# Performance work log

Hardware: AMD Instinct MI355X
Metric: run time of the kernel (lower is better)

The kernel has to match this reference:

```python
import jax, jax.numpy as jnp
import numpy as np

PATCH = 3
PAD = (PATCH - 1) // 2
WEIGHT = 100.0
EPS = 1e-9


def _extract_patches(fm):
    # fm: (C, H, W) -> (H*W, C*9) row i*W+j is the reflect-padded 3x3 patch at (i, j)
    C, H, W = fm.shape
    fm_pad = jnp.pad(fm, ((0, 0), (PAD, PAD), (PAD, PAD)), mode='reflect')
    shifts = [fm_pad[:, dh:dh + H, dw:dw + W] for dh in range(PATCH) for dw in range(PATCH)]
    p = jnp.stack(shifts, axis=0)            # (9, C, H, W)
    return p.reshape(PATCH * PATCH * C, H * W).T  # (HW, 9C)


def _match_fm(content_fm, style_fm):
    # content_fm, style_fm: (1, C, H, W); returns matched style fm (1,C,H,W) and idx (2,H,W)
    C, H, W = content_fm.shape[1:]
    cp = _extract_patches(content_fm[0])     # (HW, 9C) content patches (conv kernels)
    sp = _extract_patches(style_fm[0])       # (HW, 9C) style patches (conv sliding windows)
    c_norm = jnp.sqrt(jnp.sum(cp * cp, axis=1))  # kernel_norm per content location
    s_norm = jnp.sqrt(jnp.sum(sp * sp, axis=1))  # style_fm_norm per style location
    score = cp @ sp.T                            # (HW, HW) cross-correlation
    score = score / (c_norm[:, None] * s_norm[None, :] + EPS)
    idx = jnp.argmax(score, axis=1)              # flat argmax == torch.argmax on (H,W) map
    style_flat = style_fm[0].reshape(C, H * W)
    corr = style_flat[:, idx].reshape(1, C, H, W)  # gather matched style pixels
    corr_idx = jnp.stack([idx // W, idx % W], axis=0).reshape(2, H, W)
    return corr, corr_idx


def _masked_gram(fm, mask_flat, mask_sum):
    # fm: (1, C, H, W), mask_flat: (HW,) -> (C, C) gram of masked fm / sum(mask)
    C = fm.shape[1]
    f = fm[0].reshape(C, -1) * mask_flat[None, :]
    return (f @ f.T) / mask_sum


def setup_inputs() -> dict:
    key = jax.random.key(0)
    k1, k2, k3, k4 = jax.random.split(key, 4)
    B, C, H, W = 1, 512, 64, 64
    return {
        'content_fm': jax.random.normal(k1, (B, C, H, W), dtype=jnp.float32),
        'style_fm': jax.random.normal(k2, (B, C, H, W), dtype=jnp.float32),
        'input_fm': jax.random.normal(k3, (B, C, H, W), dtype=jnp.float32),
        'mask': jax.random.uniform(k4, (B, 1, H, W), dtype=jnp.float32),
    }


def reference(content_fm, style_fm, input_fm, mask):
    H, W = content_fm.shape[2:]
    mask_flat = mask[0, 0].reshape(H * W)
    mask_sum = jnp.sum(mask)
    # capture_style_ref: patch-match style fm to content fm, build target gram
    corr_fm, _ = _match_fm(content_fm, style_fm)
    target_gram = _masked_gram(corr_fm, mask_flat, mask_sum)
    # loss mode: masked gram of current image fm vs target, MSE (mean) * weight
    G = _masked_gram(input_fm, mask_flat, mask_sum)
    loss = jnp.mean((G - target_gram) ** 2) * WEIGHT
    return loss
```

## Files before the change

kernel.cpp:

```cpp
#include <hip/hip_runtime.h>

static constexpr int C  = 512;
static constexpr int P  = 4096;

typedef _Float16 half8  __attribute__((ext_vector_type(8)));
typedef float    f32x4  __attribute__((ext_vector_type(4)));

__device__ __forceinline__ int refl(int q) { return q < 0 ? 1 : (q > 63 ? 62 : q); }

__device__ __forceinline__ void g2l16(const void* g, const void* l) {
    __builtin_amdgcn_global_load_lds((const __attribute__((address_space(1))) unsigned int*)g,
                                     (__attribute__((address_space(3))) unsigned int*)l, 16, 0, 0);
}

__global__ __launch_bounds__(256) void k_prep(const float* __restrict__ content, const float* __restrict__ style,
                                              _Float16* __restrict__ Ah, _Float16* __restrict__ Bh,
                                              float* __restrict__ sqn_part, float* __restrict__ msum) {
    __shared__ float T[64][65];
    __shared__ float R4[4][64];
    if (blockIdx.x == 0 && threadIdx.x == 0) msum[0] = 0.f;
    const int p0 = (blockIdx.x & 63) * 64, c0 = (blockIdx.x >> 6) * 64;
    const int pl = threadIdx.x & 63, cq = threadIdx.x >> 6;
    const int pv = threadIdx.x >> 3;
    const int cv = (threadIdx.x & 7) * 8;

    #pragma unroll
    for (int r = 0; r < 16; ++r)
        T[cq + r * 4][pl] = content[(size_t)(c0 + cq + r * 4) * P + p0 + pl];
    __syncthreads();
    #pragma unroll
    for (int r = 0; r < 2; ++r) {
        int pl2 = pv + r * 32;
        half8 v;
        #pragma unroll
        for (int u = 0; u < 8; ++u) v[u] = (_Float16)T[cv + u][pl2];
        *(half8*)(Ah + (size_t)(p0 + pl2) * C + c0 + cv) = v;
    }
    __syncthreads();

    float sq = 0.f;
    #pragma unroll
    for (int r = 0; r < 16; ++r) {
        float v = style[(size_t)(c0 + cq + r * 4) * P + p0 + pl];
        T[cq + r * 4][pl] = v;
        sq += v * v;
    }
    R4[cq][pl] = sq;
    __syncthreads();
    if (cq == 0)
        sqn_part[(size_t)(blockIdx.x >> 6) * P + p0 + pl] = R4[0][pl] + R4[1][pl] + R4[2][pl] + R4[3][pl];
    #pragma unroll
    for (int r = 0; r < 2; ++r) {
        int pl2 = pv + r * 32;
        half8 v;
        #pragma unroll
        for (int u = 0; u < 8; ++u) v[u] = (_Float16)T[cv + u][pl2];
        *(half8*)(Bh + (size_t)(p0 + pl2) * C + c0 + cv) = v;
    }
}

__global__ __launch_bounds__(512, 2) void k_gemm16(const _Float16* __restrict__ Ah,
                                                   const _Float16* __restrict__ Bh,
                                                   float* __restrict__ Eo,
                                                   const float* __restrict__ sqn_part,
                                                   const float* __restrict__ mask,
                                                   float* __restrict__ inv_sn,
                                                   float* __restrict__ msum) {
    __shared__ _Float16 SH[65536];
    const int tid = threadIdx.x;
    const int bid = blockIdx.x;
    const int swz = (bid & 7) * 32 + (bid >> 3);
    const int by = swz >> 4, bx = swz & 15;

    {
        float* fsh = (float*)SH;
        const int jw0 = (bid * 16) & 63;
        const int ihh = (bid * 16) >> 6;
        if (tid < 432) {
            const int k = tid & 7, idx = tid >> 3;
            const int t3 = idx / 18, s = idx % 18;
            const int gr = refl(ihh - 1 + t3);
            const int jw = refl(jw0 - 1 + s);
            fsh[tid] = sqn_part[(size_t)k * P + gr * 64 + jw];
        }
        if (tid >= 480 && tid < 496) fsh[432 + tid - 480] = mask[bid * 16 + (tid - 480)];
        __syncthreads();
        if (tid < 54) {
            float s = fsh[tid * 8];
            #pragma unroll
            for (int k = 1; k < 8; ++k) s += fsh[tid * 8 + k];
            fsh[448 + tid] = s;
        }
        __syncthreads();
        if (tid < 16) {
            const float* sq = fsh + 448;
            float s2 = 0.f;
            #pragma unroll
            for (int t3 = 0; t3 < 3; ++t3)
                #pragma unroll
                for (int dd = 0; dd < 3; ++dd)
                    s2 += sq[t3 * 18 + tid + dd];
            inv_sn[bid * 16 + tid] = 1.0f / sqrtf(s2);
        }
        if (tid == 63) {
            float s = fsh[432];
            #pragma unroll
            for (int i = 1; i < 16; ++i) s += fsh[432 + i];
            atomicAdd(msum, s);
        }
        __syncthreads();
    }

    const int wave = tid >> 6, lane = tid & 63;
    const int wr = wave >> 2, wc = wave & 3;
    const int quad = lane >> 4, l15 = lane & 15;
    const int i0 = by * 256, j0 = bx * 256;

    const int r2 = tid >> 2;
    const int gofs = ((tid & 3) ^ (r2 & 3)) * 8;
    const _Float16* pA0 = Ah + (size_t)(i0 + r2) * C + gofs;
    const _Float16* pA1 = pA0 + (size_t)128 * C;
    const _Float16* pB0 = Bh + (size_t)(j0 + r2) * C + gofs;
    const _Float16* pB1 = pB0 + (size_t)128 * C;
    const int stw0 = wave * 512;
    const int stw1 = 4096 + wave * 512;

    const int aslot = (quad ^ (l15 & 3)) * 8;
    int aoff[8], boff[4];
    #pragma unroll
    for (int mi = 0; mi < 8; ++mi) aoff[mi] = (wr * 128 + mi * 16 + l15) * 32 + aslot;
    #pragma unroll
    for (int ni = 0; ni < 4; ++ni) boff[ni] = (wc * 64 + ni * 16 + l15) * 32 + aslot;

    f32x4 acc[8][4] = {};
    half8 af[8], bf0, bf1, bf2, bf3;

#define LDSA(b,k) (SH + (b) * 16384 + (k) * 8192)
#define LDSB(b,k) (SH + 32768 + (b) * 16384 + (k) * 8192)
#define STAGE_A(b,k,KC) do { g2l16(pA0 + (KC) + (k) * 32, LDSA(b,k) + stw0); \
                             g2l16(pA1 + (KC) + (k) * 32, LDSA(b,k) + stw1); } while (0)
#define STAGE_B(b,k,KC) do { g2l16(pB0 + (KC) + (k) * 32, LDSB(b,k) + stw0); \
                             g2l16(pB1 + (KC) + (k) * 32, LDSB(b,k) + stw1); } while (0)
#define READ_NP0(b,k) do { _Pragma("unroll") for (int mi = 0; mi < 8; ++mi) \
                               af[mi] = *(const half8*)(LDSA(b,k) + aoff[mi]); \
                           bf0 = *(const half8*)(LDSB(b,k) + boff[0]); \
                           bf1 = *(const half8*)(LDSB(b,k) + boff[1]); } while (0)
#define READ_NP1(b,k) do { bf2 = *(const half8*)(LDSB(b,k) + boff[2]); \
                           bf3 = *(const half8*)(LDSB(b,k) + boff[3]); } while (0)
#define MF8(BF,NI) do { _Pragma("unroll") for (int mi = 0; mi < 8; ++mi) \
    acc[mi][NI] = __builtin_amdgcn_mfma_f32_16x16x32_f16(af[mi], BF, acc[mi][NI], 0, 0, 0); } while (0)
#define WAITV4 asm volatile("s_waitcnt vmcnt(4)" ::: "memory")
#define WAITV0 asm volatile("s_waitcnt vmcnt(0)" ::: "memory")
#define EXEC16(B0,N0,B1,N1) do { \
    __builtin_amdgcn_s_barrier(); \
    asm volatile("s_waitcnt lgkmcnt(0)" ::: "memory"); \
    __builtin_amdgcn_sched_barrier(0); \
    __builtin_amdgcn_s_setprio(1); \
    MF8(B0, N0); MF8(B1, N1); \
    __builtin_amdgcn_s_setprio(0); \
    __builtin_amdgcn_s_barrier(); } while (0)

    STAGE_A(0, 0, 0); STAGE_B(0, 0, 0); STAGE_A(0, 1, 0); STAGE_B(0, 1, 0);
    WAITV4;
    __builtin_amdgcn_s_barrier();

    for (int it = 0; it < 4; ++it) {
        const int kk = it * 128;
        const bool nl = (it < 3);
        READ_NP0(0, 0); STAGE_A(1, 0, kk + 64);          EXEC16(bf0, 0, bf1, 1);
        READ_NP1(0, 0); STAGE_B(1, 0, kk + 64); WAITV4;  EXEC16(bf2, 2, bf3, 3);
        READ_NP0(0, 1); STAGE_A(1, 1, kk + 64);          EXEC16(bf0, 0, bf1, 1);
        READ_NP1(0, 1); STAGE_B(1, 1, kk + 64); WAITV4;  EXEC16(bf2, 2, bf3, 3);
        READ_NP0(1, 0); if (nl) STAGE_A(0, 0, kk + 128);
        EXEC16(bf0, 0, bf1, 1);
        READ_NP1(1, 0); if (nl) { STAGE_B(0, 0, kk + 128); WAITV4; } else { WAITV0; }
        EXEC16(bf2, 2, bf3, 3);
        READ_NP0(1, 1); if (nl) STAGE_A(0, 1, kk + 128);
        EXEC16(bf0, 0, bf1, 1);
        READ_NP1(1, 1); if (nl) { STAGE_B(0, 1, kk + 128); WAITV4; }
        EXEC16(bf2, 2, bf3, 3);
    }

#undef LDSA
#undef LDSB
#undef STAGE_A
#undef STAGE_B
#undef READ_NP0
#undef READ_NP1
#undef MF8
#undef WAITV4
#undef WAITV0
#undef EXEC16

    float* SHF = (float*)SH;
    __syncthreads();
    #pragma unroll
    for (int h = 0; h < 2; ++h) {
        if (wr == h) {
            #pragma unroll
            for (int mi = 0; mi < 8; ++mi) {
                const int row = mi * 16 + quad * 4;
                #pragma unroll
                for (int ni = 0; ni < 4; ++ni) {
                    float* W = SHF + row * 131 + wc * 64 + ni * 16 + l15;
                    W[0]   = acc[mi][ni][0];
                    W[131] = acc[mi][ni][1];
                    W[262] = acc[mi][ni][2];
                    W[393] = acc[mi][ni][3];
                }
            }
        }
        __syncthreads();
        {
            const int er  = tid >> 2;
            const int c00 = (tid & 3) * 8;
            const int ew  = er & 63;
            const int rm  = (er & 64) | (ew == 0 ? 1 : ew - 1);
            const int rp  = (er & 64) | (ew == 63 ? 62 : ew + 1);
            const float* Rm = SHF + rm * 131;
            const float* Rc = SHF + er * 131;
            const float* Rp = SHF + rp * 131;
            float* outRow = Eo + (size_t)(i0 + h * 128 + er) * P + j0;
            #pragma unroll
            for (int cc = 0; cc < 256; cc += 32) {
                const int cb  = c00 + cc;
                const int cw0 = cb & 63;
                f32x4 w0, w1;
                #pragma unroll
                for (int u = 0; u < 8; ++u) {
                    int cm = cb - 1 + u, cp = cb + 1 + u;
                    if (u == 0 && cw0 == 0)  cm = cb + 1;
                    if (u == 7 && cw0 == 56) cp = cb + 6;
                    float ev = Rm[cm] + Rc[cb + u] + Rp[cp];
                    if (u < 4) w0[u] = ev; else w1[u - 4] = ev;
                }
                *(f32x4*)(outRow + cb)     = w0;
                *(f32x4*)(outRow + cb + 4) = w1;
            }
        }
        if (h == 0) __syncthreads();
    }
}

__global__ __launch_bounds__(256) void k_argmax(const float* __restrict__ E,
                                                const float* __restrict__ inv_sn,
                                                int* __restrict__ idxOut) {
    const int i = blockIdx.x;
    const int ih = i >> 6, iw = i & 63;
    const int wave = threadIdx.x >> 6, l = threadIdx.x & 63, l15 = l & 15;
    size_t rb0 = (size_t)(refl(ih - 1) * 64 + iw) * P;
    size_t rb1 = (size_t)(ih * 64 + iw) * P;
    size_t rb2 = (size_t)(refl(ih + 1) * 64 + iw) * P;

    float best = -1e30f;
    int bidx = 0;
    #pragma unroll
    for (int s = 0; s < 4; ++s) {
        const int j0 = (wave * 4 + s) * 256 + l * 4;
        const int jh = j0 >> 6, jw0 = l15 * 4;
        const int cb0 = ((jh == 0) ? 1 : jh - 1) * 64 + jw0;
        const int cb1 = jh * 64 + jw0;
        const int cb2 = ((jh == 63) ? 62 : jh + 1) * 64 + jw0;
        f32x4 u0 = *(const f32x4*)(E + rb0 + cb0);
        f32x4 u1 = *(const f32x4*)(E + rb1 + cb1);
        f32x4 u2 = *(const f32x4*)(E + rb2 + cb2);
        float f0 = u0[0] + u1[0] + u2[0];
        float f1 = u0[1] + u1[1] + u2[1];
        float f2 = u0[2] + u1[2] + u2[2];
        float f3 = u0[3] + u1[3] + u2[3];
        const float4 is = *(const float4*)(inv_sn + j0);
        float v0 = f0 * is.x, v1 = f1 * is.y, v2 = f2 * is.z, v3 = f3 * is.w;
        if (v0 > best) { best = v0; bidx = j0; }
        if (v1 > best) { best = v1; bidx = j0 + 1; }
        if (v2 > best) { best = v2; bidx = j0 + 2; }
        if (v3 > best) { best = v3; bidx = j0 + 3; }
    }

    __shared__ float bv[256];
    __shared__ int   bi[256];
    bv[threadIdx.x] = best;
    bi[threadIdx.x] = bidx;
    __syncthreads();
    for (int t = 128; t > 0; t >>= 1) {
        if (threadIdx.x < t) {
            float ov = bv[threadIdx.x + t];
            int   oi = bi[threadIdx.x + t];
            if (ov > bv[threadIdx.x] || (ov == bv[threadIdx.x] && oi < bi[threadIdx.x])) {
                bv[threadIdx.x] = ov;
                bi[threadIdx.x] = oi;
            }
        }
        __syncthreads();
    }
    if (threadIdx.x == 0) idxOut[i] = bi[0];
}

__global__ __launch_bounds__(256) void k_build(const _Float16* __restrict__ Bh,
                                               const float* __restrict__ input,
                                               const float* __restrict__ mask,
                                               const int* __restrict__ idx,
                                               _Float16* __restrict__ fc, _Float16* __restrict__ fg) {
    __shared__ _Float16 G[16][520];
    __shared__ float mk[16];
    const int p0 = blockIdx.x * 16;
    const int wave = threadIdx.x >> 6, lane = threadIdx.x & 63;

    {
        int e0 = (blockIdx.x * 256 + threadIdx.x) * 32;
        #pragma unroll
        for (int v = 0; v < 4; ++v) {
            int e = e0 + v * 8;
            int pp = e & (P - 1);
            half8 vg;
            #pragma unroll
            for (int u = 0; u < 8; ++u)
                vg[u] = (_Float16)(input[e + u] * mask[pp + u]);
            *(half8*)(fg + e) = vg;
        }
    }

    if (threadIdx.x < 16) mk[threadIdx.x] = mask[p0 + threadIdx.x];

    #pragma unroll
    for (int r = 0; r < 4; ++r) {
        int pp = wave * 4 + r;
        int row = idx[p0 + pp];
        *(half8*)(&G[pp][lane * 8]) = *(const half8*)(Bh + (size_t)row * C + lane * 8);
    }
    __syncthreads();

    #pragma unroll
    for (int h = 0; h < 2; ++h) {
        int c = h * 256 + threadIdx.x;
        half8 o[2];
        #pragma unroll
        for (int q = 0; q < 2; ++q)
            #pragma unroll
            for (int u = 0; u < 8; ++u) {
                int p = q * 8 + u;
                o[q][u] = (_Float16)((float)G[p][c] * mk[p]);
            }
        _Float16* dst = fc + (size_t)c * P + p0;
        *(half8*)(dst)     = o[0];
        *(half8*)(dst + 8) = o[1];
    }
}

__device__ __constant__ int TBX[10] = {0, 0, 1, 0, 1, 2, 0, 1, 2, 3};
__device__ __constant__ int TBY[10] = {0, 1, 1, 2, 2, 2, 3, 3, 3, 3};

__global__ __launch_bounds__(256) void k_gram(const _Float16* __restrict__ fg,
                                              const _Float16* __restrict__ fc,
                                              float* __restrict__ part) {
    const int t = blockIdx.x, z = blockIdx.z;
    const int p0 = z * 256;
    const int wave = threadIdx.x >> 6, lane = threadIdx.x & 63;
    const int wr = wave >> 1, wc = wave & 1, quad = lane >> 4, l15 = lane & 15;
    const int a0 = TBY[t] * 128 + wr * 64, b0 = TBX[t] * 128 + wc * 64;

    f32x4 accg[4][4] = {};
    f32x4 accc[4][4] = {};
    for (int ks = 0; ks < 256; ks += 32) {
        int kbase = p0 + ks + quad * 8;
        half8 af[4], bf[4];
        #pragma unroll
        for (int mi = 0; mi < 4; ++mi) af[mi] = *(const half8*)(fg + (size_t)(a0 + mi * 16 + l15) * P + kbase);
        #pragma unroll
        for (int ni = 0; ni < 4; ++ni) bf[ni] = *(const half8*)(fg + (size_t)(b0 + ni * 16 + l15) * P + kbase);
        #pragma unroll
        for (int mi = 0; mi < 4; ++mi)
            #pragma unroll
            for (int ni = 0; ni < 4; ++ni)
                accg[mi][ni] = __builtin_amdgcn_mfma_f32_16x16x32_f16(af[mi], bf[ni], accg[mi][ni], 0, 0, 0);
        #pragma unroll
        for (int mi = 0; mi < 4; ++mi) af[mi] = *(const half8*)(fc + (size_t)(a0 + mi * 16 + l15) * P + kbase);
        #pragma unroll
        for (int ni = 0; ni < 4; ++ni) bf[ni] = *(const half8*)(fc + (size_t)(b0 + ni * 16 + l15) * P + kbase);
        #pragma unroll
        for (int mi = 0; mi < 4; ++mi)
            #pragma unroll
            for (int ni = 0; ni < 4; ++ni)
                accc[mi][ni] = __builtin_amdgcn_mfma_f32_16x16x32_f16(af[mi], bf[ni], accc[mi][ni], 0, 0, 0);
    }
    float* dst = part + (size_t)(z * 10 + t) * 16384;
    #pragma unroll
    for (int mi = 0; mi < 4; ++mi)
        #pragma unroll
        for (int ni = 0; ni < 4; ++ni)
            #pragma unroll
            for (int r = 0; r < 4; ++r)
                dst[(wr * 64 + mi * 16 + quad * 4 + r) * 128 + wc * 64 + ni * 16 + l15]
                    = accg[mi][ni][r] - accc[mi][ni][r];
}

__global__ void k_loss(const float* __restrict__ part, float* __restrict__ lsum) {
    int e = blockIdx.x * 256 + threadIdx.x;
    int t = e >> 14, loc = e & 16383;
    float d = 0.f;
    #pragma unroll
    for (int z = 0; z < 16; ++z) d += part[(size_t)(z * 10 + t) * 16384 + loc];
    float w = (TBX[t] == TBY[t]) ? 1.0f : 2.0f;
    __shared__ float red[256];
    red[threadIdx.x] = d * d * w;
    __syncthreads();
    for (int s = 128; s > 0; s >>= 1) {
        if (threadIdx.x < s) red[threadIdx.x] += red[threadIdx.x + s];
        __syncthreads();
    }
    if (threadIdx.x == 0) lsum[blockIdx.x] = red[0];
}

__global__ void k_final(const float* __restrict__ lsum, const float* __restrict__ msum,
                        float* __restrict__ out) {
    __shared__ float red[256];
    float s = 0.f;
    for (int e = threadIdx.x; e < 640; e += 256) s += lsum[e];
    red[threadIdx.x] = s;
    __syncthreads();
    for (int t = 128; t > 0; t >>= 1) {
        if (threadIdx.x < t) red[threadIdx.x] += red[threadIdx.x + t];
        __syncthreads();
    }
    if (threadIdx.x == 0) {
        float m = msum[0];
        out[0] = red[0] * 100.0f / (m * m * 262144.0f);
    }
}

extern "C" void kernel_launch(void* const* d_in, const int* in_sizes, int n_in,
                              void* d_out, int out_size, void* d_ws, size_t ws_size,
                              hipStream_t stream) {
    (void)in_sizes; (void)n_in; (void)out_size; (void)ws_size;
    const float* content = (const float*)d_in[0];
    const float* style   = (const float*)d_in[1];
    const float* input   = (const float*)d_in[2];
    const float* mask    = (const float*)d_in[3];

    char* ws = (char*)d_ws;
    float*    Eb   = (float*)ws;
    float*    part = (float*)ws;
    _Float16* Ah   = (_Float16*)(ws + (64u << 20));
    _Float16* Bh   = (_Float16*)(ws + (68u << 20));
    _Float16* fg_h = (_Float16*)(ws + (72u << 20));
    _Float16* fc_h = (_Float16*)(ws + (76u << 20));
    float*    small = (float*)(ws + (80u << 20));
    float* sqn_part = small;
    float* inv_sn   = small + 32768;
    float* msum     = small + 36864;
    float* lsum     = small + 36992;
    int*   idx      = (int*)(small + 37888);
    float* out = (float*)d_out;

    k_prep  <<<512, 256, 0, stream>>>(content, style, Ah, Bh, sqn_part, msum);
    k_gemm16<<<256, 512, 0, stream>>>(Ah, Bh, Eb, sqn_part, mask, inv_sn, msum);
    k_argmax<<<4096, 256, 0, stream>>>(Eb, inv_sn, idx);
    k_build <<<256, 256, 0, stream>>>(Bh, input, mask, idx, fc_h, fg_h);
    k_gram  <<<dim3(10, 1, 16), 256, 0, stream>>>(fg_h, fc_h, part);
    k_loss  <<<640, 256, 0, stream>>>(part, lsum);
    k_final <<<1, 256, 0, stream>>>(lsum, msum, out);
}
```

Measured before the change: 152.7 us.

## Halve GEMM tile height and shrink LDS staging to double occupancy

The score GEMM tile shrinks from 256x256 to 128x256 and the K-step drops to a single 32-wide slice per double-buffered stage. This cuts LDS use from 128KB to 48KB so the grid can run twice as many blocks (512) with up to four blocks per CU. The epilogue is redone as four passes over 64x128 subtiles. The aim is better latency hiding and CU fill, at the cost of less data reuse per tile, more barriers per K step, and a full vmcnt(0) wait every step.

```diff
diff --git a/kernel.cpp b/kernel.cpp
--- a/kernel.cpp
+++ b/kernel.cpp
@@ -59,20 +59,20 @@
     }
 }
 
-__global__ __launch_bounds__(512, 2) void k_gemm16(const _Float16* __restrict__ Ah,
+__global__ __launch_bounds__(512, 4) void k_gemm16(const _Float16* __restrict__ Ah,
                                                    const _Float16* __restrict__ Bh,
                                                    float* __restrict__ Eo,
                                                    const float* __restrict__ sqn_part,
                                                    const float* __restrict__ mask,
                                                    float* __restrict__ inv_sn,
                                                    float* __restrict__ msum) {
-    __shared__ _Float16 SH[65536];
+    __shared__ _Float16 SH[24576];
     const int tid = threadIdx.x;
     const int bid = blockIdx.x;
-    const int swz = (bid & 7) * 32 + (bid >> 3);
+    const int swz = (bid & 7) * 64 + (bid >> 3);
     const int by = swz >> 4, bx = swz & 15;
 
-    {
+    if (bid < 256) {
         float* fsh = (float*)SH;
         const int jw0 = (bid * 16) & 63;
         const int ihh = (bid * 16) >> 6;
@@ -114,95 +114,92 @@
     const int wave = tid >> 6, lane = tid & 63;
     const int wr = wave >> 2, wc = wave & 3;
     const int quad = lane >> 4, l15 = lane & 15;
-    const int i0 = by * 256, j0 = bx * 256;
+    const int i0 = by * 128, j0 = bx * 256;
 
     const int r2 = tid >> 2;
     const int gofs = ((tid & 3) ^ (r2 & 3)) * 8;
-    const _Float16* pA0 = Ah + (size_t)(i0 + r2) * C + gofs;
-    const _Float16* pA1 = pA0 + (size_t)128 * C;
+    const _Float16* pA  = Ah + (size_t)(i0 + r2) * C + gofs;
     const _Float16* pB0 = Bh + (size_t)(j0 + r2) * C + gofs;
     const _Float16* pB1 = pB0 + (size_t)128 * C;
-    const int stw0 = wave * 512;
-    const int stw1 = 4096 + wave * 512;
+    const int stw = wave * 512;
 
     const int aslot = (quad ^ (l15 & 3)) * 8;
-    int aoff[8], boff[4];
-    #pragma unroll
-    for (int mi = 0; mi < 8; ++mi) aoff[mi] = (wr * 128 + mi * 16 + l15) * 32 + aslot;
-    #pragma unroll
-    for (int ni = 0; ni < 4; ++ni) boff[ni] = (wc * 64 + ni * 16 + l15) * 32 + aslot;
-
-    f32x4 acc[8][4] = {};
-    half8 af[8], bf0, bf1, bf2, bf3;
-
-#define LDSA(b,k) (SH + (b) * 16384 + (k) * 8192)
-#define LDSB(b,k) (SH + 32768 + (b) * 16384 + (k) * 8192)
-#define STAGE_A(b,k,KC) do { g2l16(pA0 + (KC) + (k) * 32, LDSA(b,k) + stw0); \
-                             g2l16(pA1 + (KC) + (k) * 32, LDSA(b,k) + stw1); } while (0)
-#define STAGE_B(b,k,KC) do { g2l16(pB0 + (KC) + (k) * 32, LDSB(b,k) + stw0); \
-                             g2l16(pB1 + (KC) + (k) * 32, LDSB(b,k) + stw1); } while (0)
-#define READ_NP0(b,k) do { _Pragma("unroll") for (int mi = 0; mi < 8; ++mi) \
-                               af[mi] = *(const half8*)(LDSA(b,k) + aoff[mi]); \
-                           bf0 = *(const half8*)(LDSB(b,k) + boff[0]); \
-                           bf1 = *(const half8*)(LDSB(b,k) + boff[1]); } while (0)
-#define READ_NP1(b,k) do { bf2 = *(const half8*)(LDSB(b,k) + boff[2]); \
-                           bf3 = *(const half8*)(LDSB(b,k) + boff[3]); } while (0)
-#define MF8(BF,NI) do { _Pragma("unroll") for (int mi = 0; mi < 8; ++mi) \
+    int aoff[4], boff[4];
+    #pragma unroll
+    for (int mi = 0; mi < 4; ++mi) aoff[mi] = (wr * 64 + mi * 16 + l15) * 32 + aslot;
+    #pragma unroll
+    for (int ni = 0; ni < 4; ++ni) boff[ni] = 4096 + (wc * 64 + ni * 16 + l15) * 32 + aslot;
+
+    f32x4 acc[4][4] = {};
+    half8 af[4], bf0, bf1, bf2, bf3;
+
+#define BUF(b) (SH + (b) * 12288)
+#define STAGE_A(b,KC) g2l16(pA + (KC), BUF(b) + stw)
+#define STAGE_B(b,KC) do { g2l16(pB0 + (KC), BUF(b) + 4096 + stw); \
+                           g2l16(pB1 + (KC), BUF(b) + 8192 + stw); } while (0)
+#define READ0(b) do { _Pragma("unroll") for (int mi = 0; mi < 4; ++mi) \
+                          af[mi] = *(const half8*)(BUF(b) + aoff[mi]); \
+                      bf0 = *(const half8*)(BUF(b) + boff[0]); \
+                      bf1 = *(const half8*)(BUF(b) + boff[1]); } while (0)
+#define READ1(b) do { bf2 = *(const half8*)(BUF(b) + boff[2]); \
+                      bf3 = *(const half8*)(BUF(b) + boff[3]); } while (0)
+#define MF4(BF,NI) do { _Pragma("unroll") for (int mi = 0; mi < 4; ++mi) \
     acc[mi][NI] = __builtin_amdgcn_mfma_f32_16x16x32_f16(af[mi], BF, acc[mi][NI], 0, 0, 0); } while (0)
-#define WAITV4 asm volatile("s_waitcnt vmcnt(4)" ::: "memory")
 #define WAITV0 asm volatile("s_waitcnt vmcnt(0)" ::: "memory")
-#define EXEC16(B0,N0,B1,N1) do { \
+#define EXEC8(B0,N0,B1,N1) do { \
     __builtin_amdgcn_s_barrier(); \
     asm volatile("s_waitcnt lgkmcnt(0)" ::: "memory"); \
     __builtin_amdgcn_sched_barrier(0); \
     __builtin_amdgcn_s_setprio(1); \
-    MF8(B0, N0); MF8(B1, N1); \
+    MF4(B0, N0); MF4(B1, N1); \
     __builtin_amdgcn_s_setprio(0); \
     __builtin_amdgcn_s_barrier(); } while (0)
-
-    STAGE_A(0, 0, 0); STAGE_B(0, 0, 0); STAGE_A(0, 1, 0); STAGE_B(0, 1, 0);
-    WAITV4;
+#define EXEC8W(B0,N0,B1,N1) do { \
+    __builtin_amdgcn_s_barrier(); \
+    asm volatile("s_waitcnt lgkmcnt(0)" ::: "memory"); \
+    __builtin_amdgcn_sched_barrier(0); \
+    __builtin_amdgcn_s_setprio(1); \
+    MF4(B0, N0); MF4(B1, N1); \
+    __builtin_amdgcn_s_setprio(0); \
+    WAITV0; \
+    __builtin_amdgcn_s_barrier(); } while (0)
+
+    STAGE_A(0, 0); STAGE_B(0, 0);
+    WAITV0;
     __builtin_amdgcn_s_barrier();
 
-    for (int it = 0; it < 4; ++it) {
-        const int kk = it * 128;
-        const bool nl = (it < 3);
-        READ_NP0(0, 0); STAGE_A(1, 0, kk + 64);          EXEC16(bf0, 0, bf1, 1);
-        READ_NP1(0, 0); STAGE_B(1, 0, kk + 64); WAITV4;  EXEC16(bf2, 2, bf3, 3);
-        READ_NP0(0, 1); STAGE_A(1, 1, kk + 64);          EXEC16(bf0, 0, bf1, 1);
-        READ_NP1(0, 1); STAGE_B(1, 1, kk + 64); WAITV4;  EXEC16(bf2, 2, bf3, 3);
-        READ_NP0(1, 0); if (nl) STAGE_A(0, 0, kk + 128);
-        EXEC16(bf0, 0, bf1, 1);
-        READ_NP1(1, 0); if (nl) { STAGE_B(0, 0, kk + 128); WAITV4; } else { WAITV0; }
-        EXEC16(bf2, 2, bf3, 3);
-        READ_NP0(1, 1); if (nl) STAGE_A(0, 1, kk + 128);
-        EXEC16(bf0, 0, bf1, 1);
-        READ_NP1(1, 1); if (nl) { STAGE_B(0, 1, kk + 128); WAITV4; }
-        EXEC16(bf2, 2, bf3, 3);
-    }
-
-#undef LDSA
-#undef LDSB
+    #pragma unroll 2
+    for (int t = 0; t < 16; ++t) {
+        const int b = t & 1;
+        const int kn = (t + 1) * 32;
+        READ0(b); if (t < 15) STAGE_A(b ^ 1, kn);
+        EXEC8(bf0, 0, bf1, 1);
+        READ1(b); if (t < 15) STAGE_B(b ^ 1, kn);
+        EXEC8W(bf2, 2, bf3, 3);
+    }
+
+#undef BUF
 #undef STAGE_A
 #undef STAGE_B
-#undef READ_NP0
-#undef READ_NP1
-#undef MF8
-#undef WAITV4
+#undef READ0
+#undef READ1
+#undef MF4
 #undef WAITV0
-#undef EXEC16
+#undef EXEC8
+#undef EXEC8W
 
     float* SHF = (float*)SH;
     __syncthreads();
     #pragma unroll
-    for (int h = 0; h < 2; ++h) {
-        if (wr == h) {
-            #pragma unroll
-            for (int mi = 0; mi < 8; ++mi) {
+    for (int pass = 0; pass < 4; ++pass) {
+        const int p = pass >> 1, ch = pass & 1;
+        if (wr == p && (wc >> 1) == ch) {
+            #pragma unroll
+            for (int mi = 0; mi < 4; ++mi) {
                 const int row = mi * 16 + quad * 4;
                 #pragma unroll
                 for (int ni = 0; ni < 4; ++ni) {
-                    float* W = SHF + row * 131 + wc * 64 + ni * 16 + l15;
+                    float* W = SHF + row * 131 + (wc & 1) * 64 + ni * 16 + l15;
                     W[0]   = acc[mi][ni][0];
                     W[131] = acc[mi][ni][1];
                     W[262] = acc[mi][ni][2];
@@ -212,17 +209,16 @@
         }
         __syncthreads();
         {
-            const int er  = tid >> 2;
-            const int c00 = (tid & 3) * 8;
-            const int ew  = er & 63;
-            const int rm  = (er & 64) | (ew == 0 ? 1 : ew - 1);
-            const int rp  = (er & 64) | (ew == 63 ? 62 : ew + 1);
+            const int er  = tid >> 3;
+            const int c00 = (tid & 7) * 16;
+            const int rm  = (er == 0) ? 1 : er - 1;
+            const int rp  = (er == 63) ? 62 : er + 1;
             const float* Rm = SHF + rm * 131;
             const float* Rc = SHF + er * 131;
             const float* Rp = SHF + rp * 131;
-            float* outRow = Eo + (size_t)(i0 + h * 128 + er) * P + j0;
-            #pragma unroll
-            for (int cc = 0; cc < 256; cc += 32) {
+            float* outRow = Eo + (size_t)(i0 + p * 64 + er) * P + j0 + ch * 128;
+            #pragma unroll
+            for (int cc = 0; cc < 16; cc += 8) {
                 const int cb  = c00 + cc;
                 const int cw0 = cb & 63;
                 f32x4 w0, w1;
@@ -238,7 +234,7 @@
                 *(f32x4*)(outRow + cb + 4) = w1;
             }
         }
-        if (h == 0) __syncthreads();
+        if (pass < 3) __syncthreads();
     }
 }
 
@@ -452,7 +448,7 @@
     float* out = (float*)d_out;
 
     k_prep  <<<512, 256, 0, stream>>>(content, style, Ah, Bh, sqn_part, msum);
-    k_gemm16<<<256, 512, 0, stream>>>(Ah, Bh, Eb, sqn_part, mask, inv_sn, msum);
+    k_gemm16<<<512, 512, 0, stream>>>(Ah, Bh, Eb, sqn_part, mask, inv_sn, msum);
     k_argmax<<<4096, 256, 0, stream>>>(Eb, inv_sn, idx);
     k_build <<<256, 256, 0, stream>>>(Bh, input, mask, idx, fc_h, fg_h);
     k_gram  <<<dim3(10, 1, 16), 256, 0, stream>>>(fg_h, fc_h, part);
```

Result: slower. 162.0 us (+6.0%).
